# Kernel optimization log

Hardware: AMD Instinct MI355X
Metric: run time of the kernel (lower is better)

## Reference

```python
import jax, jax.numpy as jnp
import numpy as np

B, H, S, D = 2, 16, 2048, 64
MASK_NEG = 1e9


def setup_inputs() -> dict:
    key = jax.random.key(0)
    kq, kk, kv, km = jax.random.split(key, 4)
    Q = jax.random.normal(kq, (B, H, S, D), dtype=jnp.float32)
    K = jax.random.normal(kk, (B, H, S, D), dtype=jnp.float32)
    V = jax.random.normal(kv, (B, H, S, D), dtype=jnp.float32)
    # float 0/1 mask, broadcast over heads; 1 = masked-out position
    attn_mask = jax.random.randint(km, (B, 1, S, S), 0, 2).astype(jnp.float32)
    return {"Q": Q, "K": K, "V": V, "attn_mask": attn_mask}


def reference(Q, K, V, attn_mask):
    # scores: [B, H, S, S]
    attn_score = jnp.einsum('bhqd,bhkd->bhqk', Q, K)
    scale = jnp.sqrt(jnp.asarray(K.shape[-1], dtype=jnp.float32))
    attn_scale = attn_score / scale - MASK_NEG * attn_mask
    attn_prob = jax.nn.softmax(attn_scale, axis=-1)
    attn_out = jnp.einsum('bhqk,bhkd->bhqd', attn_prob, V)
    return attn_out
```

## Files before the change

kernel.cpp:

```cpp
#include <hip/hip_runtime.h>


#define S_LEN 2048
#define D_DIM 64
#define WPR   32
#define NIT   32

typedef __attribute__((ext_vector_type(8))) short bf16x8;
typedef __attribute__((ext_vector_type(4))) float f32x4;
typedef unsigned long long ull;

__device__ __forceinline__ f32x4 mfma16(bf16x8 a, bf16x8 b, f32x4 c) {
  return __builtin_amdgcn_mfma_f32_16x16x32_bf16(a, b, c, 0, 0, 0);
}
__device__ __forceinline__ unsigned short f2bf(float f) {
  unsigned u = __builtin_bit_cast(unsigned, f);
  unsigned r = u + 0x7FFFu + ((u >> 16) & 1u);
  return (unsigned short)(r >> 16);
}
__device__ __forceinline__ float bf2f(unsigned short s) {
  unsigned u = ((unsigned)s) << 16;
  return __builtin_bit_cast(float, u);
}
__device__ __forceinline__ float fexp2(float x) {
#if __has_builtin(__builtin_amdgcn_exp2f)
  return __builtin_amdgcn_exp2f(x);
#else
  return exp2f(x);
#endif
}
__device__ __forceinline__ bool detect_bf16(const void* maskp) {
  const unsigned short* s = (const unsigned short*)maskp;
  unsigned short v = s[2 * (threadIdx.x & 63)];
  return __ballot(v == (unsigned short)0x3F80) != 0ull;
}
__device__ __forceinline__ int4 cvt_f8(const float* p) {
  float4 f0 = *(const float4*)p;
  float4 f1 = *(const float4*)(p + 4);
  int4 r;
  r.x = (unsigned)f2bf(f0.x) | ((unsigned)f2bf(f0.y) << 16);
  r.y = (unsigned)f2bf(f0.z) | ((unsigned)f2bf(f0.w) << 16);
  r.z = (unsigned)f2bf(f1.x) | ((unsigned)f2bf(f1.y) << 16);
  r.w = (unsigned)f2bf(f1.z) | ((unsigned)f2bf(f1.w) << 16);
  return r;
}

#define C1 0.18033688011112042f
#define C2 1.4426950408889634e9f

__global__ __launch_bounds__(256) void prep_all(
    const void* __restrict__ M, const void* __restrict__ Kin,
    const void* __restrict__ Vin, ull* __restrict__ bits,
    unsigned short* __restrict__ Kf, unsigned short* __restrict__ Vf) {
  __shared__ __align__(16) unsigned short T[64 * 72];
  const bool isb = detect_bf16(M);
  const unsigned bx = blockIdx.x;
  const int tid = threadIdx.x;

  if (bx < 32768u) {
    unsigned idx = bx * 256u + tid;
    bool on = isb ? (bf2f(((const unsigned short*)M)[idx]) > 0.5f)
                  : (((const float*)M)[idx] > 0.5f);
    ull bm = __ballot(on);
    if ((tid & 63) == 0) {
      unsigned c = idx & 2047u, r = (idx >> 11) & 2047u, bb = idx >> 22;
      bits[(((size_t)(bb * WPR + (c >> 6))) << 11) + r] = bm;
    }
  } else if (bx < 32768u + 2048u) {
    unsigned g = (bx - 32768u) * 256u + tid;
    unsigned lane = g & 63u;
    unsigned f = (g >> 6) & 7u;
    unsigned ti = (g >> 9) & 31u;
    unsigned bh = g >> 14;
    unsigned nt = f >> 1, kt = f & 1;
    unsigned quad = lane >> 4, l15 = lane & 15;
    size_t src = (size_t)bh * (S_LEN * D_DIM) +
                 (size_t)(ti * 64 + nt * 16 + l15) * D_DIM + kt * 32 + quad * 8;
    int4 out;
    if (isb) out = *(const int4*)((const unsigned short*)Kin + src);
    else     out = cvt_f8((const float*)Kin + src);
    *(int4*)&Kf[(size_t)g * 8] = out;
  } else {
    unsigned idx = bx - (32768u + 2048u);
    unsigned bh = idx >> 5, ti = idx & 31u;
    {
      int k = tid >> 2, d0 = (tid & 3) * 16;
      size_t src = (size_t)bh * (S_LEN * D_DIM) + (size_t)(ti * 64 + k) * D_DIM + d0;
      int4 a, c;
      if (isb) {
        const unsigned short* s = (const unsigned short*)Vin + src;
        a = *(const int4*)s; c = *(const int4*)(s + 8);
      } else {
        const float* s = (const float*)Vin + src;
        a = cvt_f8(s); c = cvt_f8(s + 8);
      }
      *(int4*)&T[k * 72 + d0] = a;
      *(int4*)&T[k * 72 + d0 + 8] = c;
    }
    __syncthreads();
    #pragma unroll
    for (int h = 0; h < 2; ++h) {
      int c = tid + h * 256;
      int lane = c & 63, f = c >> 6;
      int kt = f >> 2, nt = f & 3;
      int quad = lane >> 4, l15 = lane & 15;
      unsigned short v[8];
      #pragma unroll
      for (int j = 0; j < 8; ++j)
        v[j] = T[(kt * 32 + quad * 8 + j) * 72 + nt * 16 + l15];
      *(int4*)&Vf[(((size_t)(bh * 32 + ti)) * 8 + f) * 512 + lane * 8] = *(int4*)v;
    }
  }
}

__global__ __launch_bounds__(256, 4) void attn_fast(
    const void* __restrict__ Qp, const unsigned short* __restrict__ Kf,
    const unsigned short* __restrict__ Vf, const ull* __restrict__ bits,
    const void* __restrict__ maskp, void* __restrict__ Op) {
  __shared__ __align__(16) unsigned short Plds[4 * 32 * 72];
  __shared__ __align__(16) f32x4 Lcomb[2][8];

  const bool isb = detect_bf16(maskp);
  const int tid  = threadIdx.x;
  const int wave = tid >> 6;
  const int lane = tid & 63;
  const int l15  = lane & 15;
  const int quad = lane >> 4;
  const int pair = wave >> 1;
  const int half = wave & 1;
  const int q0   = blockIdx.x * 64;
  const int bh   = blockIdx.y;
  const int b    = bh >> 4;
  const size_t base = (size_t)bh * S_LEN * D_DIM;
  const int rows0 = q0 + pair * 32;

  bf16x8 qf[2][2];
  #pragma unroll
  for (int mi = 0; mi < 2; ++mi)
    #pragma unroll
    for (int kt = 0; kt < 2; ++kt) {
      size_t off = base + (size_t)(rows0 + mi * 16 + l15) * D_DIM + kt * 32 + quad * 8;
      unsigned short v[8];
      if (isb) {
        *(int4*)v = *(const int4*)((const unsigned short*)Qp + off);
        #pragma unroll
        for (int j = 0; j < 8; ++j) v[j] = f2bf(bf2f(v[j]) * C1);
      } else {
        const float* f = (const float*)Qp + off;
        float4 f0 = *(const float4*)f;
        float4 f1 = *(const float4*)(f + 4);
        v[0] = f2bf(f0.x * C1); v[1] = f2bf(f0.y * C1);
        v[2] = f2bf(f0.z * C1); v[3] = f2bf(f0.w * C1);
        v[4] = f2bf(f1.x * C1); v[5] = f2bf(f1.y * C1);
        v[6] = f2bf(f1.z * C1); v[7] = f2bf(f1.w * C1);
      }
      qf[mi][kt] = *(const bf16x8*)v;
    }

  f32x4 acc_o[2][4];
  f32x4 acc_l[2];
  const f32x4 zero4 = {0.f, 0.f, 0.f, 0.f};
  #pragma unroll
  for (int mi = 0; mi < 2; ++mi) {
    acc_l[mi] = zero4;
    #pragma unroll
    for (int nt = 0; nt < 4; ++nt) acc_o[mi][nt] = zero4;
  }
  bf16x8 onesB;
  {
    short ov = (l15 == 0) ? (short)0x3F80 : (short)0;
    #pragma unroll
    for (int i = 0; i < 8; ++i) onesB[i] = ov;
  }

  unsigned short* Pw = Plds + wave * (32 * 72);
  const int it0 = half * 16;

  for (int it = it0; it < it0 + 16; ++it) {
    const unsigned short* Kb = Kf + (((size_t)(bh * 32 + it)) * 8) * 512 + lane * 8;
    const unsigned short* Vb = Vf + (((size_t)(bh * 32 + it)) * 8) * 512 + lane * 8;
    bf16x8 kfr[4][2], vfr[2][4];
    #pragma unroll
    for (int nt = 0; nt < 4; ++nt)
      #pragma unroll
      for (int kt = 0; kt < 2; ++kt)
        kfr[nt][kt] = *(const bf16x8*)(Kb + (nt * 2 + kt) * 512);
    #pragma unroll
    for (int kt = 0; kt < 2; ++kt)
      #pragma unroll
      for (int nt = 0; nt < 4; ++nt)
        vfr[kt][nt] = *(const bf16x8*)(Vb + (kt * 4 + nt) * 512);

    unsigned mlo[2][4], mhi[2][4];
    {
      const ull* bw = bits + (((size_t)(b * WPR + it)) << 11) + rows0;
      #pragma unroll
      for (int mi = 0; mi < 2; ++mi) {
        ulonglong2 a = *(const ulonglong2*)(bw + mi * 16 + quad * 4);
        ulonglong2 c = *(const ulonglong2*)(bw + mi * 16 + quad * 4 + 2);
        ull w0 = a.x >> l15, w1 = a.y >> l15, w2 = c.x >> l15, w3 = c.y >> l15;
        mlo[mi][0] = (unsigned)w0; mhi[mi][0] = (unsigned)(w0 >> 32);
        mlo[mi][1] = (unsigned)w1; mhi[mi][1] = (unsigned)(w1 >> 32);
        mlo[mi][2] = (unsigned)w2; mhi[mi][2] = (unsigned)(w2 >> 32);
        mlo[mi][3] = (unsigned)w3; mhi[mi][3] = (unsigned)(w3 >> 32);
      }
    }

    #pragma unroll
    for (int nt = 0; nt < 4; ++nt) {
      f32x4 s0 = zero4, s1 = zero4;
      s0 = mfma16(qf[0][0], kfr[nt][0], s0);
      s0 = mfma16(qf[0][1], kfr[nt][1], s0);
      s1 = mfma16(qf[1][0], kfr[nt][0], s1);
      s1 = mfma16(qf[1][1], kfr[nt][1], s1);
      #pragma unroll
      for (int mi = 0; mi < 2; ++mi) {
        f32x4 sv = mi ? s1 : s0;
        #pragma unroll
        for (int reg = 0; reg < 4; ++reg) {
          float p = fexp2(sv[reg]);
          unsigned bit = (nt < 2) ? ((mlo[mi][reg] >> (nt * 16)) & 1u)
                                  : ((mhi[mi][reg] >> ((nt - 2) * 16)) & 1u);
          if (bit) p = 0.0f;
          Pw[(mi * 16 + quad * 4 + reg) * 72 + nt * 16 + l15] = (short)f2bf(p);
        }
      }
    }

    #pragma unroll
    for (int kt = 0; kt < 2; ++kt) {
      bf16x8 pf0 = *(const bf16x8*)&Pw[(l15) * 72 + kt * 32 + quad * 8];
      bf16x8 pf1 = *(const bf16x8*)&Pw[(16 + l15) * 72 + kt * 32 + quad * 8];
      #pragma unroll
      for (int nt = 0; nt < 4; ++nt) {
        acc_o[0][nt] = mfma16(pf0, vfr[kt][nt], acc_o[0][nt]);
        acc_o[1][nt] = mfma16(pf1, vfr[kt][nt], acc_o[1][nt]);
      }
      acc_l[0] = mfma16(pf0, onesB, acc_l[0]);
      acc_l[1] = mfma16(pf1, onesB, acc_l[1]);
    }
  }

  __syncthreads();
  f32x4* Pc = (f32x4*)Plds;
  if (half == 1) {
    #pragma unroll
    for (int mi = 0; mi < 2; ++mi) {
      #pragma unroll
      for (int nt = 0; nt < 4; ++nt)
        Pc[(size_t)(pair * 8 + mi * 4 + nt) * 64 + lane] = acc_o[mi][nt];
      if (l15 == 0) Lcomb[pair][mi * 4 + quad] = acc_l[mi];
    }
  }
  __syncthreads();
  if (half == 0) {
    #pragma unroll
    for (int mi = 0; mi < 2; ++mi) {
      #pragma unroll
      for (int nt = 0; nt < 4; ++nt)
        acc_o[mi][nt] += Pc[(size_t)(pair * 8 + mi * 4 + nt) * 64 + lane];
      #pragma unroll
      for (int reg = 0; reg < 4; ++reg) {
        float lv = __shfl(acc_l[mi][reg], lane & 48, 64) + Lcomb[pair][mi * 4 + quad][reg];
        float inv = 1.0f / lv;
        #pragma unroll
        for (int nt = 0; nt < 4; ++nt) {
          float o = acc_o[mi][nt][reg] * inv;
          size_t idx = base + (size_t)(rows0 + mi * 16 + quad * 4 + reg) * D_DIM + nt * 16 + l15;
          if (isb) ((unsigned short*)Op)[idx] = f2bf(o);
          else     ((float*)Op)[idx] = o;
        }
      }
    }
  }
}

__global__ __launch_bounds__(256, 2) void attn_fallback(
    const void* __restrict__ Qp, const void* __restrict__ Kp,
    const void* __restrict__ Vp, const void* __restrict__ maskp,
    void* __restrict__ Op) {
  __shared__ __align__(16) short QKlds[128 * 72];
  __shared__ __align__(16) short Vtlds[64 * 72];
  __shared__ __align__(16) short Plds2[128 * 72];

  const bool isb = detect_bf16(maskp);
  const int tid  = threadIdx.x;
  const int wave = tid >> 6;
  const int lane = tid & 63;
  const int l15  = lane & 15;
  const int quad = lane >> 4;
  const int q0   = blockIdx.x * 128;
  const int bh   = blockIdx.y;
  const int b    = bh >> 4;
  const size_t base = (size_t)bh * S_LEN * D_DIM;

  const short* Qs = (const short*)Qp; const float* Qf = (const float*)Qp;
  const short* Ks = (const short*)Kp; const float* Kf2 = (const float*)Kp;
  const short* Vs = (const short*)Vp; const float* Vf2 = (const float*)Vp;

  if (isb) {
    const short* Qg = Qs + base + (size_t)q0 * D_DIM;
    #pragma unroll
    for (int p = 0; p < 4; ++p) {
      int e = p * 2048 + tid * 8;
      *(int4*)&QKlds[(e >> 6) * 72 + (e & 63)] = *(const int4*)(Qg + e);
    }
  } else {
    const float* Qg = Qf + base + (size_t)q0 * D_DIM;
    #pragma unroll
    for (int p = 0; p < 4; ++p) {
      int e = p * 2048 + tid * 8;
      *(int4*)&QKlds[(e >> 6) * 72 + (e & 63)] = cvt_f8(Qg + e);
    }
  }
  __syncthreads();
  bf16x8 qf[2][2];
  #pragma unroll
  for (int mi = 0; mi < 2; ++mi)
    #pragma unroll
    for (int kt = 0; kt < 2; ++kt)
      qf[mi][kt] = *(const bf16x8*)&QKlds[(wave * 32 + mi * 16 + l15) * 72 + kt * 32 + quad * 8];
  __syncthreads();

  f32x4 acc_o[2][4];
  f32x4 acc_l[2];
  const f32x4 zero4 = {0.f, 0.f, 0.f, 0.f};
  #pragma unroll
  for (int mi = 0; mi < 2; ++mi) {
    acc_l[mi] = zero4;
    #pragma unroll
    for (int nt = 0; nt < 4; ++nt) acc_o[mi][nt] = zero4;
  }
  bf16x8 onesB;
  {
    short ov = (l15 == 0) ? (short)0x3F80 : (short)0;
    #pragma unroll
    for (int i = 0; i < 8; ++i) onesB[i] = ov;
  }

  for (int it = 0; it < NIT; ++it) {
    const int k0 = it * 64;
    if (isb) {
      const short* Kg = Ks + base + (size_t)k0 * D_DIM;
      #pragma unroll
      for (int p = 0; p < 2; ++p) {
        int e = p * 2048 + tid * 8;
        *(int4*)&QKlds[(e >> 6) * 72 + (e & 63)] = *(const int4*)(Kg + e);
      }
    } else {
      const float* Kg = Kf2 + base + (size_t)k0 * D_DIM;
      #pragma unroll
      for (int p = 0; p < 2; ++p) {
        int e = p * 2048 + tid * 8;
        *(int4*)&QKlds[(e >> 6) * 72 + (e & 63)] = cvt_f8(Kg + e);
      }
    }
    {
      const int r0 = (tid >> 3) * 2;
      const int d0 = (tid & 7) * 8;
      unsigned short as_[8], bs_[8];
      if (isb) {
        const short* Vg = Vs + base + (size_t)k0 * D_DIM;
        *(int4*)as_ = *(const int4*)(Vg + r0 * D_DIM + d0);
        *(int4*)bs_ = *(const int4*)(Vg + (r0 + 1) * D_DIM + d0);
      } else {
        const float* Vg = Vf2 + base + (size_t)k0 * D_DIM;
        *(int4*)as_ = cvt_f8(Vg + r0 * D_DIM + d0);
        *(int4*)bs_ = cvt_f8(Vg + (r0 + 1) * D_DIM + d0);
      }
      #pragma unroll
      for (int j = 0; j < 8; ++j) {
        int d = d0 + j;
        int blk = (r0 >> 3) ^ (d >> 3);
        unsigned pk = (unsigned)as_[j] | ((unsigned)bs_[j] << 16);
        *(unsigned*)&Vtlds[d * 72 + blk * 8 + (r0 & 7)] = pk;
      }
    }
    __syncthreads();

    f32x4 sc[2][4];
    #pragma unroll
    for (int mi = 0; mi < 2; ++mi)
      #pragma unroll
      for (int nt = 0; nt < 4; ++nt) sc[mi][nt] = zero4;
    #pragma unroll
    for (int nt = 0; nt < 4; ++nt) {
      bf16x8 kf0 = *(const bf16x8*)&QKlds[(nt * 16 + l15) * 72 + quad * 8];
      bf16x8 kf1 = *(const bf16x8*)&QKlds[(nt * 16 + l15) * 72 + 32 + quad * 8];
      #pragma unroll
      for (int mi = 0; mi < 2; ++mi) {
        sc[mi][nt] = mfma16(qf[mi][0], kf0, sc[mi][nt]);
        sc[mi][nt] = mfma16(qf[mi][1], kf1, sc[mi][nt]);
      }
    }

    #pragma unroll
    for (int mi = 0; mi < 2; ++mi) {
      #pragma unroll
      for (int nt = 0; nt < 4; ++nt) {
        #pragma unroll
        for (int reg = 0; reg < 4; ++reg) {
          int rg = q0 + wave * 32 + mi * 16 + quad * 4 + reg;
          size_t mix = (size_t)b * S_LEN * S_LEN + (size_t)rg * S_LEN + k0 + nt * 16 + l15;
          float mv = isb ? bf2f(((const unsigned short*)maskp)[mix])
                         : ((const float*)maskp)[mix];
          float y = sc[mi][nt][reg] * C1 - mv * C2;
          Plds2[(wave * 32 + mi * 16 + quad * 4 + reg) * 72 + nt * 16 + l15] =
              (short)f2bf(fexp2(y));
        }
      }
    }
    __syncthreads();

    #pragma unroll
    for (int kt = 0; kt < 2; ++kt) {
      bf16x8 pf[2];
      #pragma unroll
      for (int mi = 0; mi < 2; ++mi)
        pf[mi] = *(const bf16x8*)&Plds2[(wave * 32 + mi * 16 + l15) * 72 + kt * 32 + quad * 8];
      #pragma unroll
      for (int nt = 0; nt < 4; ++nt) {
        int d = nt * 16 + l15;
        int kb = (kt * 4 + quad) ^ (d >> 3);
        bf16x8 vf = *(const bf16x8*)&Vtlds[d * 72 + kb * 8];
        #pragma unroll
        for (int mi = 0; mi < 2; ++mi)
          acc_o[mi][nt] = mfma16(pf[mi], vf, acc_o[mi][nt]);
      }
      #pragma unroll
      for (int mi = 0; mi < 2; ++mi)
        acc_l[mi] = mfma16(pf[mi], onesB, acc_l[mi]);
    }
    __syncthreads();
  }

  #pragma unroll
  for (int mi = 0; mi < 2; ++mi) {
    #pragma unroll
    for (int reg = 0; reg < 4; ++reg) {
      float lv = __shfl(acc_l[mi][reg], lane & 48, 64);
      float inv = 1.0f / lv;
      #pragma unroll
      for (int nt = 0; nt < 4; ++nt) {
        float o = acc_o[mi][nt][reg] * inv;
        size_t idx = base + (size_t)(q0 + wave * 32 + mi * 16 + quad * 4 + reg) * D_DIM + nt * 16 + l15;
        if (isb) ((unsigned short*)Op)[idx] = f2bf(o);
        else     ((float*)Op)[idx] = o;
      }
    }
  }
}

extern "C" void kernel_launch(void* const* d_in, const int* in_sizes, int n_in,
                              void* d_out, int out_size, void* d_ws, size_t ws_size,
                              hipStream_t stream) {
  const void* Q = d_in[0];
  const void* K = d_in[1];
  const void* V = d_in[2];
  const void* M = d_in[3];

  dim3 block(256);
  const size_t bits_bytes = (size_t)2 * S_LEN * S_LEN / 8;
  const size_t tens_bytes = (size_t)2 * 16 * S_LEN * D_DIM * 2;

  if (ws_size >= bits_bytes + 2 * tens_bytes) {
    char* ws = (char*)d_ws;
    ull* bits = (ull*)ws;
    unsigned short* Kf = (unsigned short*)(ws + bits_bytes);
    unsigned short* Vf = (unsigned short*)(ws + bits_bytes + tens_bytes);
    prep_all<<<dim3(32768 + 2048 + 1024), block, 0, stream>>>(M, K, V, bits, Kf, Vf);
    attn_fast<<<dim3(S_LEN / 64, 32), block, 0, stream>>>(Q, Kf, Vf, bits, M, d_out);
  } else {
    attn_fallback<<<dim3(S_LEN / 128, 32), block, 0, stream>>>(Q, K, V, M, d_out);
  }
}
```

Before: 190.5 us.

## Switch attention to 32x32 MFMA with register-resident P and 4-way KV split

The fast attention kernel now uses 32x32x16 bf16 MFMA tiles and computes S transposed (K as the A operand), so probabilities stay in registers. They are repacked with ds_bpermute instead of being written to and read back from LDS. Each block handles 32 query rows, with four waves splitting the KV range and combining partial results through LDS at the end. The K/V pre-layout kernel is changed to match the new fragment layout, and a packed bf16 conversion intrinsic is used where available. This removes the LDS round-trip for P and increases grid size, but adds a four-way reduction with several barriers and puts more pressure on registers.

```diff
diff --git a/kernel.cpp b/kernel.cpp
--- a/kernel.cpp
+++ b/kernel.cpp
@@ -6,10 +6,14 @@
 #define WPR   32
 #define NIT   32
 
-typedef __attribute__((ext_vector_type(8))) short bf16x8;
-typedef __attribute__((ext_vector_type(4))) float f32x4;
+typedef __attribute__((ext_vector_type(8)))  short bf16x8;
+typedef __attribute__((ext_vector_type(4)))  float f32x4;
+typedef __attribute__((ext_vector_type(16))) float f32x16;
 typedef unsigned long long ull;
 
+__device__ __forceinline__ f32x16 mfma32(bf16x8 a, bf16x8 b, f32x16 c) {
+  return __builtin_amdgcn_mfma_f32_32x32x16_bf16(a, b, c, 0, 0, 0);
+}
 __device__ __forceinline__ f32x4 mfma16(bf16x8 a, bf16x8 b, f32x4 c) {
   return __builtin_amdgcn_mfma_f32_16x16x32_bf16(a, b, c, 0, 0, 0);
 }
@@ -21,6 +25,19 @@
 __device__ __forceinline__ float bf2f(unsigned short s) {
   unsigned u = ((unsigned)s) << 16;
   return __builtin_bit_cast(float, u);
+}
+__device__ __forceinline__ unsigned packbf(float a, float b) {
+#if __has_builtin(__builtin_amdgcn_cvt_pk_bf16_f32)
+  typedef __bf16 bfv2 __attribute__((ext_vector_type(2)));
+  bfv2 v = __builtin_amdgcn_cvt_pk_bf16_f32(a, b);
+  return __builtin_bit_cast(unsigned, v);
+#else
+  unsigned ua = __builtin_bit_cast(unsigned, a);
+  unsigned ub = __builtin_bit_cast(unsigned, b);
+  ua = ua + 0x7FFFu + ((ua >> 16) & 1u);
+  ub = ub + 0x7FFFu + ((ub >> 16) & 1u);
+  return (ua >> 16) | (ub & 0xFFFF0000u);
+#endif
 }
 __device__ __forceinline__ float fexp2(float x) {
 #if __has_builtin(__builtin_amdgcn_exp2f)
@@ -38,10 +55,10 @@
   float4 f0 = *(const float4*)p;
   float4 f1 = *(const float4*)(p + 4);
   int4 r;
-  r.x = (unsigned)f2bf(f0.x) | ((unsigned)f2bf(f0.y) << 16);
-  r.y = (unsigned)f2bf(f0.z) | ((unsigned)f2bf(f0.w) << 16);
-  r.z = (unsigned)f2bf(f1.x) | ((unsigned)f2bf(f1.y) << 16);
-  r.w = (unsigned)f2bf(f1.z) | ((unsigned)f2bf(f1.w) << 16);
+  r.x = (int)packbf(f0.x, f0.y);
+  r.y = (int)packbf(f0.z, f0.w);
+  r.z = (int)packbf(f1.x, f1.y);
+  r.w = (int)packbf(f1.z, f1.w);
   return r;
 }
 
@@ -68,24 +85,20 @@
     }
   } else if (bx < 32768u + 2048u) {
     unsigned g = (bx - 32768u) * 256u + tid;
-    unsigned lane = g & 63u;
-    unsigned f = (g >> 6) & 7u;
-    unsigned ti = (g >> 9) & 31u;
-    unsigned bh = g >> 14;
-    unsigned nt = f >> 1, kt = f & 1;
-    unsigned quad = lane >> 4, l15 = lane & 15;
+    unsigned lane = g & 63u, f = (g >> 6) & 7u, it = (g >> 9) & 31u, bh = g >> 14;
+    unsigned t = f >> 2, dc = f & 3, hi = lane >> 5, l31 = lane & 31;
     size_t src = (size_t)bh * (S_LEN * D_DIM) +
-                 (size_t)(ti * 64 + nt * 16 + l15) * D_DIM + kt * 32 + quad * 8;
+                 (size_t)(it * 64 + t * 32 + l31) * D_DIM + dc * 16 + hi * 8;
     int4 out;
     if (isb) out = *(const int4*)((const unsigned short*)Kin + src);
     else     out = cvt_f8((const float*)Kin + src);
     *(int4*)&Kf[(size_t)g * 8] = out;
   } else {
     unsigned idx = bx - (32768u + 2048u);
-    unsigned bh = idx >> 5, ti = idx & 31u;
+    unsigned bh = idx >> 5, it = idx & 31u;
     {
       int k = tid >> 2, d0 = (tid & 3) * 16;
-      size_t src = (size_t)bh * (S_LEN * D_DIM) + (size_t)(ti * 64 + k) * D_DIM + d0;
+      size_t src = (size_t)bh * (S_LEN * D_DIM) + (size_t)(it * 64 + k) * D_DIM + d0;
       int4 a, c;
       if (isb) {
         const unsigned short* s = (const unsigned short*)Vin + src;
@@ -102,13 +115,13 @@
     for (int h = 0; h < 2; ++h) {
       int c = tid + h * 256;
       int lane = c & 63, f = c >> 6;
-      int kt = f >> 2, nt = f & 3;
-      int quad = lane >> 4, l15 = lane & 15;
+      int t = f >> 2, kc = (f >> 1) & 1, dt = f & 1;
+      int hi = lane >> 5, l31 = lane & 31;
       unsigned short v[8];
       #pragma unroll
       for (int j = 0; j < 8; ++j)
-        v[j] = T[(kt * 32 + quad * 8 + j) * 72 + nt * 16 + l15];
-      *(int4*)&Vf[(((size_t)(bh * 32 + ti)) * 8 + f) * 512 + lane * 8] = *(int4*)v;
+        v[j] = T[(t * 32 + kc * 16 + hi * 8 + j) * 72 + dt * 32 + l31];
+      *(int4*)&Vf[(((size_t)(bh * 32 + it)) * 8 + f) * 512 + lane * 8] = *(int4*)v;
     }
   }
 }
@@ -117,159 +130,156 @@
     const void* __restrict__ Qp, const unsigned short* __restrict__ Kf,
     const unsigned short* __restrict__ Vf, const ull* __restrict__ bits,
     const void* __restrict__ maskp, void* __restrict__ Op) {
-  __shared__ __align__(16) unsigned short Plds[4 * 32 * 72];
-  __shared__ __align__(16) f32x4 Lcomb[2][8];
+  __shared__ float Comb[2][32][64];
+  __shared__ float Lc[4][32];
 
   const bool isb = detect_bf16(maskp);
   const int tid  = threadIdx.x;
   const int wave = tid >> 6;
   const int lane = tid & 63;
-  const int l15  = lane & 15;
-  const int quad = lane >> 4;
-  const int pair = wave >> 1;
-  const int half = wave & 1;
-  const int q0   = blockIdx.x * 64;
+  const int hi   = lane >> 5;
+  const int l31  = lane & 31;
+  const int q0   = blockIdx.x * 32;
   const int bh   = blockIdx.y;
   const int b    = bh >> 4;
   const size_t base = (size_t)bh * S_LEN * D_DIM;
-  const int rows0 = q0 + pair * 32;
-
-  bf16x8 qf[2][2];
+  const int xidx = ((lane ^ 32) & 63) * 4;
+
+  bf16x8 qf[4];
   #pragma unroll
-  for (int mi = 0; mi < 2; ++mi)
-    #pragma unroll
-    for (int kt = 0; kt < 2; ++kt) {
-      size_t off = base + (size_t)(rows0 + mi * 16 + l15) * D_DIM + kt * 32 + quad * 8;
-      unsigned short v[8];
-      if (isb) {
-        *(int4*)v = *(const int4*)((const unsigned short*)Qp + off);
-        #pragma unroll
-        for (int j = 0; j < 8; ++j) v[j] = f2bf(bf2f(v[j]) * C1);
-      } else {
-        const float* f = (const float*)Qp + off;
-        float4 f0 = *(const float4*)f;
-        float4 f1 = *(const float4*)(f + 4);
-        v[0] = f2bf(f0.x * C1); v[1] = f2bf(f0.y * C1);
-        v[2] = f2bf(f0.z * C1); v[3] = f2bf(f0.w * C1);
-        v[4] = f2bf(f1.x * C1); v[5] = f2bf(f1.y * C1);
-        v[6] = f2bf(f1.z * C1); v[7] = f2bf(f1.w * C1);
-      }
-      qf[mi][kt] = *(const bf16x8*)v;
-    }
-
-  f32x4 acc_o[2][4];
-  f32x4 acc_l[2];
-  const f32x4 zero4 = {0.f, 0.f, 0.f, 0.f};
+  for (int dc = 0; dc < 4; ++dc) {
+    size_t off = base + (size_t)(q0 + l31) * D_DIM + dc * 16 + hi * 8;
+    float v[8];
+    if (isb) {
+      unsigned short u[8];
+      *(int4*)u = *(const int4*)((const unsigned short*)Qp + off);
+      #pragma unroll
+      for (int j = 0; j < 8; ++j) v[j] = bf2f(u[j]) * C1;
+    } else {
+      const float* f = (const float*)Qp + off;
+      float4 f0 = *(const float4*)f;
+      float4 f1 = *(const float4*)(f + 4);
+      v[0] = f0.x * C1; v[1] = f0.y * C1; v[2] = f0.z * C1; v[3] = f0.w * C1;
+      v[4] = f1.x * C1; v[5] = f1.y * C1; v[6] = f1.z * C1; v[7] = f1.w * C1;
+    }
+    uint4 d;
+    d.x = packbf(v[0], v[1]); d.y = packbf(v[2], v[3]);
+    d.z = packbf(v[4], v[5]); d.w = packbf(v[6], v[7]);
+    qf[dc] = __builtin_bit_cast(bf16x8, d);
+  }
+
+  f32x16 acc_o[2];
+  f32x16 acc_l;
   #pragma unroll
-  for (int mi = 0; mi < 2; ++mi) {
-    acc_l[mi] = zero4;
-    #pragma unroll
-    for (int nt = 0; nt < 4; ++nt) acc_o[mi][nt] = zero4;
-  }
+  for (int r = 0; r < 16; ++r) { acc_o[0][r] = 0.f; acc_o[1][r] = 0.f; acc_l[r] = 0.f; }
+
   bf16x8 onesB;
   {
-    short ov = (l15 == 0) ? (short)0x3F80 : (short)0;
+    short ov = (l31 == 0) ? (short)0x3F80 : (short)0;
     #pragma unroll
     for (int i = 0; i < 8; ++i) onesB[i] = ov;
   }
 
-  unsigned short* Pw = Plds + wave * (32 * 72);
-  const int it0 = half * 16;
-
-  for (int it = it0; it < it0 + 16; ++it) {
-    const unsigned short* Kb = Kf + (((size_t)(bh * 32 + it)) * 8) * 512 + lane * 8;
-    const unsigned short* Vb = Vf + (((size_t)(bh * 32 + it)) * 8) * 512 + lane * 8;
-    bf16x8 kfr[4][2], vfr[2][4];
-    #pragma unroll
-    for (int nt = 0; nt < 4; ++nt)
-      #pragma unroll
-      for (int kt = 0; kt < 2; ++kt)
-        kfr[nt][kt] = *(const bf16x8*)(Kb + (nt * 2 + kt) * 512);
-    #pragma unroll
-    for (int kt = 0; kt < 2; ++kt)
-      #pragma unroll
-      for (int nt = 0; nt < 4; ++nt)
-        vfr[kt][nt] = *(const bf16x8*)(Vb + (kt * 4 + nt) * 512);
-
-    unsigned mlo[2][4], mhi[2][4];
-    {
-      const ull* bw = bits + (((size_t)(b * WPR + it)) << 11) + rows0;
-      #pragma unroll
-      for (int mi = 0; mi < 2; ++mi) {
-        ulonglong2 a = *(const ulonglong2*)(bw + mi * 16 + quad * 4);
-        ulonglong2 c = *(const ulonglong2*)(bw + mi * 16 + quad * 4 + 2);
-        ull w0 = a.x >> l15, w1 = a.y >> l15, w2 = c.x >> l15, w3 = c.y >> l15;
-        mlo[mi][0] = (unsigned)w0; mhi[mi][0] = (unsigned)(w0 >> 32);
-        mlo[mi][1] = (unsigned)w1; mhi[mi][1] = (unsigned)(w1 >> 32);
-        mlo[mi][2] = (unsigned)w2; mhi[mi][2] = (unsigned)(w2 >> 32);
-        mlo[mi][3] = (unsigned)w3; mhi[mi][3] = (unsigned)(w3 >> 32);
-      }
-    }
-
-    #pragma unroll
-    for (int nt = 0; nt < 4; ++nt) {
-      f32x4 s0 = zero4, s1 = zero4;
-      s0 = mfma16(qf[0][0], kfr[nt][0], s0);
-      s0 = mfma16(qf[0][1], kfr[nt][1], s0);
-      s1 = mfma16(qf[1][0], kfr[nt][0], s1);
-      s1 = mfma16(qf[1][1], kfr[nt][1], s1);
-      #pragma unroll
-      for (int mi = 0; mi < 2; ++mi) {
-        f32x4 sv = mi ? s1 : s0;
+  for (int i = 0; i < NIT / 4; ++i) {
+    const int it = wave * (NIT / 4) + i;
+    const size_t fb = ((size_t)(bh * 32 + it)) * 8 * 512;
+
+    ull w = bits[(((size_t)(b * WPR + it)) << 11) + q0 + l31] >> (hi * 4);
+    unsigned wt[2] = {(unsigned)w, (unsigned)(w >> 32)};
+
+    #pragma unroll
+    for (int t = 0; t < 2; ++t) {
+      const unsigned short* Kb = Kf + fb + (size_t)(t * 4) * 512 + lane * 8;
+      f32x16 sc;
+      #pragma unroll
+      for (int r = 0; r < 16; ++r) sc[r] = 0.f;
+      #pragma unroll
+      for (int dc = 0; dc < 4; ++dc) {
+        bf16x8 kfr = *(const bf16x8*)(Kb + dc * 512);
+        sc = mfma32(kfr, qf[dc], sc);
+      }
+
+      float p[16];
+      #pragma unroll
+      for (int r = 0; r < 16; ++r) {
+        float e = fexp2(sc[r]);
+        unsigned bit = (wt[t] >> ((r & 3) + 8 * (r >> 2))) & 1u;
+        p[r] = bit ? 0.0f : e;
+      }
+
+      #pragma unroll
+      for (int kc = 0; kc < 2; ++kc) {
+        unsigned pk0 = packbf(p[8 * kc + 0], p[8 * kc + 1]);
+        unsigned pk1 = packbf(p[8 * kc + 2], p[8 * kc + 3]);
+        unsigned pk2 = packbf(p[8 * kc + 4], p[8 * kc + 5]);
+        unsigned pk3 = packbf(p[8 * kc + 6], p[8 * kc + 7]);
+        unsigned x0 = (unsigned)__builtin_amdgcn_ds_bpermute(xidx, (int)pk0);
+        unsigned x1 = (unsigned)__builtin_amdgcn_ds_bpermute(xidx, (int)pk1);
+        unsigned x2 = (unsigned)__builtin_amdgcn_ds_bpermute(xidx, (int)pk2);
+        unsigned x3 = (unsigned)__builtin_amdgcn_ds_bpermute(xidx, (int)pk3);
+        uint4 d;
+        d.x = hi ? x2 : pk0;
+        d.y = hi ? x3 : pk1;
+        d.z = hi ? pk2 : x0;
+        d.w = hi ? pk3 : x1;
+        bf16x8 pf = __builtin_bit_cast(bf16x8, d);
+
+        const unsigned short* Vb = Vf + fb + (size_t)(t * 4 + kc * 2) * 512 + lane * 8;
         #pragma unroll
-        for (int reg = 0; reg < 4; ++reg) {
-          float p = fexp2(sv[reg]);
-          unsigned bit = (nt < 2) ? ((mlo[mi][reg] >> (nt * 16)) & 1u)
-                                  : ((mhi[mi][reg] >> ((nt - 2) * 16)) & 1u);
-          if (bit) p = 0.0f;
-          Pw[(mi * 16 + quad * 4 + reg) * 72 + nt * 16 + l15] = (short)f2bf(p);
+        for (int dt = 0; dt < 2; ++dt) {
+          bf16x8 vfr = *(const bf16x8*)(Vb + dt * 512);
+          acc_o[dt] = mfma32(pf, vfr, acc_o[dt]);
         }
-      }
-    }
-
-    #pragma unroll
-    for (int kt = 0; kt < 2; ++kt) {
-      bf16x8 pf0 = *(const bf16x8*)&Pw[(l15) * 72 + kt * 32 + quad * 8];
-      bf16x8 pf1 = *(const bf16x8*)&Pw[(16 + l15) * 72 + kt * 32 + quad * 8];
-      #pragma unroll
-      for (int nt = 0; nt < 4; ++nt) {
-        acc_o[0][nt] = mfma16(pf0, vfr[kt][nt], acc_o[0][nt]);
-        acc_o[1][nt] = mfma16(pf1, vfr[kt][nt], acc_o[1][nt]);
-      }
-      acc_l[0] = mfma16(pf0, onesB, acc_l[0]);
-      acc_l[1] = mfma16(pf1, onesB, acc_l[1]);
-    }
-  }
-
-  __syncthreads();
-  f32x4* Pc = (f32x4*)Plds;
-  if (half == 1) {
-    #pragma unroll
-    for (int mi = 0; mi < 2; ++mi) {
-      #pragma unroll
-      for (int nt = 0; nt < 4; ++nt)
-        Pc[(size_t)(pair * 8 + mi * 4 + nt) * 64 + lane] = acc_o[mi][nt];
-      if (l15 == 0) Lcomb[pair][mi * 4 + quad] = acc_l[mi];
-    }
-  }
-  __syncthreads();
-  if (half == 0) {
-    #pragma unroll
-    for (int mi = 0; mi < 2; ++mi) {
-      #pragma unroll
-      for (int nt = 0; nt < 4; ++nt)
-        acc_o[mi][nt] += Pc[(size_t)(pair * 8 + mi * 4 + nt) * 64 + lane];
-      #pragma unroll
-      for (int reg = 0; reg < 4; ++reg) {
-        float lv = __shfl(acc_l[mi][reg], lane & 48, 64) + Lcomb[pair][mi * 4 + quad][reg];
-        float inv = 1.0f / lv;
-        #pragma unroll
-        for (int nt = 0; nt < 4; ++nt) {
-          float o = acc_o[mi][nt][reg] * inv;
-          size_t idx = base + (size_t)(rows0 + mi * 16 + quad * 4 + reg) * D_DIM + nt * 16 + l15;
-          if (isb) ((unsigned short*)Op)[idx] = f2bf(o);
-          else     ((float*)Op)[idx] = o;
-        }
+        acc_l = mfma32(pf, onesB, acc_l);
+      }
+    }
+  }
+
+  __syncthreads();
+  if (wave >= 2) {
+    #pragma unroll
+    for (int dt = 0; dt < 2; ++dt)
+      #pragma unroll
+      for (int r = 0; r < 16; ++r)
+        Comb[wave - 2][dt * 16 + r][lane] = acc_o[dt][r];
+  }
+  if (l31 == 0) {
+    #pragma unroll
+    for (int r = 0; r < 16; ++r)
+      Lc[wave][(r & 3) + 8 * (r >> 2) + 4 * hi] = acc_l[r];
+  }
+  __syncthreads();
+  if (wave < 2) {
+    #pragma unroll
+    for (int dt = 0; dt < 2; ++dt)
+      #pragma unroll
+      for (int r = 0; r < 16; ++r)
+        acc_o[dt][r] += Comb[wave][dt * 16 + r][lane];
+  }
+  __syncthreads();
+  if (wave == 1) {
+    #pragma unroll
+    for (int dt = 0; dt < 2; ++dt)
+      #pragma unroll
+      for (int r = 0; r < 16; ++r)
+        Comb[0][dt * 16 + r][lane] = acc_o[dt][r];
+  }
+  __syncthreads();
+  if (wave == 0) {
+    #pragma unroll
+    for (int r = 0; r < 16; ++r) {
+      int m = (r & 3) + 8 * (r >> 2) + 4 * hi;
+      float o0 = acc_o[0][r] + Comb[0][r][lane];
+      float o1 = acc_o[1][r] + Comb[0][16 + r][lane];
+      float lv = Lc[0][m] + Lc[1][m] + Lc[2][m] + Lc[3][m];
+      float inv = 1.0f / lv;
+      size_t idx = base + (size_t)(q0 + m) * D_DIM + l31;
+      if (isb) {
+        ((unsigned short*)Op)[idx]      = f2bf(o0 * inv);
+        ((unsigned short*)Op)[idx + 32] = f2bf(o1 * inv);
+      } else {
+        ((float*)Op)[idx]      = o0 * inv;
+        ((float*)Op)[idx + 32] = o1 * inv;
       }
     }
   }
@@ -469,7 +479,7 @@
     unsigned short* Kf = (unsigned short*)(ws + bits_bytes);
     unsigned short* Vf = (unsigned short*)(ws + bits_bytes + tens_bytes);
     prep_all<<<dim3(32768 + 2048 + 1024), block, 0, stream>>>(M, K, V, bits, Kf, Vf);
-    attn_fast<<<dim3(S_LEN / 64, 32), block, 0, stream>>>(Q, Kf, Vf, bits, M, d_out);
+    attn_fast<<<dim3(S_LEN / 32, 32), block, 0, stream>>>(Q, Kf, Vf, bits, M, d_out);
   } else {
     attn_fallback<<<dim3(S_LEN / 128, 32), block, 0, stream>>>(Q, K, V, M, d_out);
   }
```

After: 192.4 us. Within noise of the previous version (+1.0%).
